# Performance work log

Measured on AMD Instinct MI355X. Metric: run time of the kernel, lower is better.

The kernel has to match this reference:

```python
import jax, jax.numpy as jnp
import numpy as np

ALPHA = 0.1  # history blend factor from __init__


def _grid_sample_border(tex_t, grid):
    """Bilinear grid_sample, align_corners=False, padding_mode='border'.
    tex_t: [N,H,W,C] (channels-last), grid: [N,Hg,Wg,2] with (x,y) in [-1,1].
    Returns [N,Hg,Wg,C].
    """
    N, H, W, C = tex_t.shape
    x = (grid[..., 0] + 1.0) * (W * 0.5) - 0.5  # pixel coords
    y = (grid[..., 1] + 1.0) * (H * 0.5) - 0.5
    x0f = jnp.floor(x)
    y0f = jnp.floor(y)
    wx = (x - x0f)[..., None]
    wy = (y - y0f)[..., None]
    x0 = jnp.clip(x0f.astype(jnp.int32), 0, W - 1)
    x1 = jnp.clip(x0f.astype(jnp.int32) + 1, 0, W - 1)
    y0 = jnp.clip(y0f.astype(jnp.int32), 0, H - 1)
    y1 = jnp.clip(y0f.astype(jnp.int32) + 1, 0, H - 1)
    b = jnp.arange(N)[:, None, None]
    v00 = tex_t[b, y0, x0]
    v01 = tex_t[b, y0, x1]
    v10 = tex_t[b, y1, x0]
    v11 = tex_t[b, y1, x1]
    top = v00 * (1.0 - wx) + v01 * wx
    bot = v10 * (1.0 - wx) + v11 * wx
    return top * (1.0 - wy) + bot * wy


def _bicubic_grid_sample(tex, grid):
    """Catmull-Rom 5-tap bicubic sampling (matches torch BiCubicGridSample).
    tex: [N,C,H,W], grid: [N,Hg,Wg,2]. Returns [N,C,Hg,Wg].
    The torch code appends an all-ones alpha channel before weighting; since
    bilinear sampling of a constant-1 channel is 1, the alpha accumulator
    equals the sum of the 5 scalar weights, which we compute directly.
    """
    N, C, H, W = tex.shape
    tex_t = jnp.transpose(tex, (0, 2, 3, 1))  # NHWC
    ws = jnp.array([W, H], dtype=tex.dtype)
    rws = 1.0 / ws
    uv = (grid + 1.0) * 0.5
    pos = uv * ws
    cpos = jnp.floor(pos - 0.5) + 0.5
    f = pos - cpos
    f2 = f * f
    f3 = f2 * f
    w0 = -0.5 * f3 + f2 - 0.5 * f
    w2 = -1.5 * f3 + 2.0 * f2 + 0.5 * f
    w3 = 0.5 * f3 - 0.5 * f2
    w12 = (1.5 * f3 - 2.5 * f2 + 1.0) + w2  # w1 + w2
    tc12 = rws * (cpos + w2 / w12)
    tc0 = rws * (cpos - 1.0)
    tc3 = rws * (cpos + 2.0)

    def samp(uvx, uvy):
        g = (jnp.stack([uvx, uvy], axis=-1) - 0.5) * 2.0
        return _grid_sample_border(tex_t, g)  # [N,Hg,Wg,C]

    # scalar per-pixel weights
    ww1 = w12[..., 0] * w0[..., 1]
    ww2 = w0[..., 0] * w12[..., 1]
    ww3 = w3[..., 0] * w12[..., 1]
    ww4 = w12[..., 0] * w3[..., 1]
    ww5 = w12[..., 0] * w12[..., 1]

    out = (samp(tc12[..., 0], tc0[..., 1]) * ww1[..., None]
           + samp(tc0[..., 0], tc12[..., 1]) * ww2[..., None]
           + samp(tc3[..., 0], tc12[..., 1]) * ww3[..., None]
           + samp(tc12[..., 0], tc3[..., 1]) * ww4[..., None]
           + samp(tc12[..., 0], tc12[..., 1]) * ww5[..., None])
    rec = (ww1 + ww2 + ww3 + ww4 + ww5)[..., None]
    out = out / rec
    return jnp.transpose(out, (0, 3, 1, 2))  # NCHW


def _max_pool3(x):
    # 3x3 max pool, stride 1, padding 1 on NCHW
    return jax.lax.reduce_window(x, -jnp.inf, jax.lax.max,
                                 (1, 1, 3, 3), (1, 1, 1, 1), 'SAME')


def setup_inputs() -> dict:
    key = jax.random.key(0)
    k1, k2, k3 = jax.random.split(key, 3)
    N, C, H, W = 2, 3, 1080, 1920
    x = jax.random.uniform(k1, (N, C, H, W), dtype=jnp.float32)
    history = jax.random.uniform(k2, (N, C, H, W), dtype=jnp.float32)
    # motion-vector grid: roughly identity UVs with small per-pixel jitter
    gy, gx = jnp.meshgrid(
        (jnp.arange(H, dtype=jnp.float32) + 0.5) / H * 2.0 - 1.0,
        (jnp.arange(W, dtype=jnp.float32) + 0.5) / W * 2.0 - 1.0,
        indexing='ij')
    base = jnp.stack([gx, gy], axis=-1)[None]  # [1,H,W,2]
    jitter = (jax.random.uniform(k3, (N, H, W, 2), dtype=jnp.float32) - 0.5) * 0.01
    mv = base + jitter
    return {"x": x, "mv": mv, "history": history}


def reference(x, mv, history):
    reproj = _bicubic_grid_sample(history, mv)
    max_nh = _max_pool3(x)
    min_nh = -_max_pool3(-x)
    reproj = jnp.minimum(jnp.maximum(reproj, min_nh), max_nh)
    return ALPHA * x + (1.0 - ALPHA) * reproj
```

## Files before the change

kernel.cpp:

```cpp
#include <hip/hip_runtime.h>

static constexpr float ALPHA = 0.1f;

#define TW 64
#define TH 8
#define HROWS 16
#define HCOLS 84
#define CHOFF (HROWS * HCOLS)

__device__ __forceinline__ int iclamp(int v, int lo, int hi) { return min(max(v, lo), hi); }

struct Setup {
    int mA, m1, m2, mB;
    float t, w0, w3, w12;
};

__device__ __forceinline__ Setup axis_setup(float gcoord, float S) {
    Setup s;
    float pos = (gcoord + 1.0f) * 0.5f * S;
    float pm  = floorf(pos - 0.5f);
    float f   = pos - (pm + 0.5f);
    float f2 = f * f, f3 = f2 * f;
    s.w0  = -0.5f * f3 + f2 - 0.5f * f;
    float w2 = -1.5f * f3 + 2.0f * f2 + 0.5f * f;
    s.w3  =  0.5f * f3 - 0.5f * f2;
    s.w12 = (1.5f * f3 - 2.5f * f2 + 1.0f) + w2;
    float p12 = pm + __fdividef(w2, s.w12);
    float fl  = floorf(p12);
    s.t = p12 - fl;
    int m = (int)pm, i12 = (int)fl;
    s.mA = m - 1; s.m1 = i12; s.m2 = i12 + 1; s.mB = m + 2;
    return s;
}

__global__ __launch_bounds__(256, 4) void taa_kernel(
    const float* __restrict__ x, const float* __restrict__ mv,
    const float* __restrict__ hist, float* __restrict__ out)
{
    constexpr int N = 2, H = 1080, W = 1920, HW = H * W;
    constexpr int NTX = W / TW;
    constexpr int NTY = H / TH;
    constexpr int NWG = N * NTX * NTY;
    constexpr int Q = NWG / 8, R = NWG % 8;

    __shared__ __align__(16) float Lh[3 * CHOFF];

    int d = blockIdx.x;
    int xcd = d & 7, di = d >> 3;
    int work = (xcd < R ? xcd * (Q + 1) : R * (Q + 1) + (xcd - R) * Q) + di;
    int n   = work / (NTX * NTY);
    int rem = work - n * (NTX * NTY);
    int ty  = rem / NTX;
    int tx  = rem - ty * NTX;
    const int w0 = tx * TW, h0 = ty * TH;

    const int lx = threadIdx.x & 63;
    const int wv = threadIdx.x >> 6;
    const int wpix = w0 + lx;
    const int hbase = h0 + 2 * wv;

    const float* hn = hist + n * 3 * HW;
    const float* xn = x    + n * 3 * HW;

    const float2 g0 = ((const float2*)mv)[n * HW + hbase * W + wpix];
    const float2 g1 = ((const float2*)mv)[n * HW + (hbase + 1) * W + wpix];

    const bool interior = (tx >= 1) && (tx <= NTX - 2) &&
                          (h0 >= 4) && (h0 + TH + 3 <= H - 1);
    if (interior) {
        float4* Lh4 = (float4*)Lh;
        for (int idx = threadIdx.x; idx < 1008; idx += 256) {
            int c  = idx / 336;
            int rm = idx - c * 336;
            int r  = rm / 21;
            int c4 = rm - r * 21;
            Lh4[idx] = *(const float4*)(hn + c * HW + (h0 - 4 + r) * W + (w0 - 8) + c4 * 4);
        }
    } else {
        for (int idx = threadIdx.x; idx < 4032; idx += 256) {
            int c  = idx / CHOFF;
            int rm = idx - c * CHOFF;
            int r  = rm / HCOLS;
            int cc = rm - r * HCOLS;
            int gr = iclamp(h0 - 4 + r, 0, H - 1);
            int gc = iclamp(w0 - 8 + cc, 0, W - 1);
            Lh[idx] = hn[c * HW + gr * W + gc];
        }
    }

    int rg0 = iclamp(hbase - 1, 0, H - 1) * W;
    int rg1 = hbase * W;
    int rg2 = (hbase + 1) * W;
    int rg3 = iclamp(hbase + 2, 0, H - 1) * W;
    const int rg[4] = {rg0, rg1, rg2, rg3};

    float hmx[3][4], hmn[3][4], xmid[3][4];
    if (tx >= 1 && tx <= NTX - 2) {
#pragma unroll
        for (int c = 0; c < 3; ++c) {
            const float* xc = xn + c * HW + wpix;
#pragma unroll
            for (int rr = 0; rr < 4; ++rr) {
                const float* p = xc + rg[rr];
                float a = p[-1], b = p[0], e = p[1];
                hmx[c][rr]  = fmaxf(fmaxf(a, b), e);
                hmn[c][rr]  = fminf(fminf(a, b), e);
                xmid[c][rr] = b;
            }
        }
    } else {
        const int wm = max(wpix - 1, 0), wp = min(wpix + 1, W - 1);
#pragma unroll
        for (int c = 0; c < 3; ++c) {
            const float* xc = xn + c * HW;
#pragma unroll
            for (int rr = 0; rr < 4; ++rr) {
                float a = xc[rg[rr] + wm];
                float b = xc[rg[rr] + wpix];
                float e = xc[rg[rr] + wp];
                hmx[c][rr]  = fmaxf(fmaxf(a, b), e);
                hmn[c][rr]  = fminf(fminf(a, b), e);
                xmid[c][rr] = b;
            }
        }
    }

    Setup sx0 = axis_setup(g0.x, (float)W);
    Setup sy0 = axis_setup(g0.y, (float)H);
    Setup sx1 = axis_setup(g1.x, (float)W);
    Setup sy1 = axis_setup(g1.y, (float)H);

    __syncthreads();

    float* on = out + n * 3 * HW;

#pragma unroll
    for (int p = 0; p < 2; ++p) {
        const Setup& sx = p ? sx1 : sx0;
        const Setup& sy = p ? sy1 : sy0;

        const int lrA = iclamp(sy.mA - (h0 - 4), 0, HROWS - 1);
        const int lr1 = iclamp(sy.m1 - (h0 - 4), 0, HROWS - 1);
        const int lr2 = iclamp(sy.m2 - (h0 - 4), 0, HROWS - 1);
        const int lrB = iclamp(sy.mB - (h0 - 4), 0, HROWS - 1);
        const int lcA = iclamp(sx.mA - (w0 - 8), 0, HCOLS - 1);
        const int lc1 = iclamp(sx.m1 - (w0 - 8), 0, HCOLS - 1);
        const int lc2 = iclamp(sx.m2 - (w0 - 8), 0, HCOLS - 1);
        const int lcB = iclamp(sx.mB - (w0 - 8), 0, HCOLS - 1);

        const int rA = lrA * HCOLS, r1 = lr1 * HCOLS, r2 = lr2 * HCOLS, rB = lrB * HCOLS;
        const int oA1 = rA + lc1, oA2 = rA + lc2;
        const int o1A = r1 + lcA, o11 = r1 + lc1, o12 = r1 + lc2, o1B = r1 + lcB;
        const int o2A = r2 + lcA, o21 = r2 + lc1, o22 = r2 + lc2, o2B = r2 + lcB;
        const int oB1 = rB + lc1, oB2 = rB + lc2;

        const float tx_ = sx.t, ty_ = sy.t;
        const float omtx = 1.0f - tx_, omty = 1.0f - ty_;
        const float ww1 = sx.w12 * sy.w0;
        const float ww2 = sx.w0  * sy.w12;
        const float ww3 = sx.w3  * sy.w12;
        const float ww4 = sx.w12 * sy.w3;
        const float ww5 = sx.w12 * sy.w12;
        const float rrec = __fdividef(1.0f, ww1 + ww2 + ww3 + ww4 + ww5);

        const int gpix = (hbase + p) * W + wpix;

#pragma unroll
        for (int c = 0; c < 3; ++c) {
            const float* L = Lh + c * CHOFF;
            float s1   = L[oA1] * omtx + L[oA2] * tx_;
            float s4   = L[oB1] * omtx + L[oB2] * tx_;
            float s2   = L[o1A] * omty + L[o2A] * ty_;
            float s3   = L[o1B] * omty + L[o2B] * ty_;
            float top5 = L[o11] * omtx + L[o12] * tx_;
            float bot5 = L[o21] * omtx + L[o22] * tx_;
            float s5   = top5 * omty + bot5 * ty_;
            float reproj = (s1 * ww1 + s2 * ww2 + s3 * ww3 + s4 * ww4 + s5 * ww5) * rrec;

            float mxv = fmaxf(fmaxf(hmx[c][p], hmx[c][p + 1]), hmx[c][p + 2]);
            float mnv = fminf(fminf(hmn[c][p], hmn[c][p + 1]), hmn[c][p + 2]);
            reproj = fminf(fmaxf(reproj, mnv), mxv);

            on[c * HW + gpix] = ALPHA * xmid[c][p + 1] + (1.0f - ALPHA) * reproj;
        }
    }
}

extern "C" void kernel_launch(void* const* d_in, const int* in_sizes, int n_in,
                              void* d_out, int out_size, void* d_ws, size_t ws_size,
                              hipStream_t stream) {
    const float* x    = (const float*)d_in[0];
    const float* mv   = (const float*)d_in[1];
    const float* hist = (const float*)d_in[2];
    float* out = (float*)d_out;

    constexpr int NWG = 2 * (1920 / TW) * (1080 / TH);
    taa_kernel<<<dim3(NWG, 1, 1), dim3(256, 1, 1), 0, stream>>>(x, mv, hist, out);
}
```

Baseline: 48.23 us.

## Interleave history channels in LDS as float4 texels for vectorized gathers

The shared-memory history tile changes from planar per-channel arrays to one padded float4 per texel holding RGB plus a zero. Each bicubic tap then costs one 128-bit LDS read instead of three scalar reads, and the interpolation runs on vectors. The cost is that global loads in the fill loop become scalar, three per texel, instead of float4 row loads. LDS footprint grows by a third for the padding, which may lower occupancy and adds bank pressure on the wide reads.

```diff
diff --git a/kernel.cpp b/kernel.cpp
--- a/kernel.cpp
+++ b/kernel.cpp
@@ -1,12 +1,14 @@
 #include <hip/hip_runtime.h>
 
 static constexpr float ALPHA = 0.1f;
+
+typedef float f4 __attribute__((ext_vector_type(4)));
 
 #define TW 64
 #define TH 8
 #define HROWS 16
 #define HCOLS 84
-#define CHOFF (HROWS * HCOLS)
+#define NTEX (HROWS * HCOLS)
 
 __device__ __forceinline__ int iclamp(int v, int lo, int hi) { return min(max(v, lo), hi); }
 
@@ -43,7 +45,7 @@
     constexpr int NWG = N * NTX * NTY;
     constexpr int Q = NWG / 8, R = NWG % 8;
 
-    __shared__ __align__(16) float Lh[3 * CHOFF];
+    __shared__ __align__(16) f4 Lh[NTEX];
 
     int d = blockIdx.x;
     int xcd = d & 7, di = d >> 3;
@@ -68,23 +70,30 @@
     const bool interior = (tx >= 1) && (tx <= NTX - 2) &&
                           (h0 >= 4) && (h0 + TH + 3 <= H - 1);
     if (interior) {
-        float4* Lh4 = (float4*)Lh;
-        for (int idx = threadIdx.x; idx < 1008; idx += 256) {
-            int c  = idx / 336;
-            int rm = idx - c * 336;
-            int r  = rm / 21;
-            int c4 = rm - r * 21;
-            Lh4[idx] = *(const float4*)(hn + c * HW + (h0 - 4 + r) * W + (w0 - 8) + c4 * 4);
+        for (int idx = threadIdx.x; idx < NTEX; idx += 256) {
+            int r  = idx / HCOLS;
+            int cc = idx - r * HCOLS;
+            const float* src = hn + (h0 - 4 + r) * W + (w0 - 8) + cc;
+            f4 t;
+            t.x = src[0];
+            t.y = src[HW];
+            t.z = src[2 * HW];
+            t.w = 0.0f;
+            Lh[idx] = t;
         }
     } else {
-        for (int idx = threadIdx.x; idx < 4032; idx += 256) {
-            int c  = idx / CHOFF;
-            int rm = idx - c * CHOFF;
-            int r  = rm / HCOLS;
-            int cc = rm - r * HCOLS;
+        for (int idx = threadIdx.x; idx < NTEX; idx += 256) {
+            int r  = idx / HCOLS;
+            int cc = idx - r * HCOLS;
             int gr = iclamp(h0 - 4 + r, 0, H - 1);
             int gc = iclamp(w0 - 8 + cc, 0, W - 1);
-            Lh[idx] = hn[c * HW + gr * W + gc];
+            const float* src = hn + gr * W + gc;
+            f4 t;
+            t.x = src[0];
+            t.y = src[HW];
+            t.z = src[2 * HW];
+            t.w = 0.0f;
+            Lh[idx] = t;
         }
     }
 
@@ -149,10 +158,13 @@
         const int lcB = iclamp(sx.mB - (w0 - 8), 0, HCOLS - 1);
 
         const int rA = lrA * HCOLS, r1 = lr1 * HCOLS, r2 = lr2 * HCOLS, rB = lrB * HCOLS;
-        const int oA1 = rA + lc1, oA2 = rA + lc2;
-        const int o1A = r1 + lcA, o11 = r1 + lc1, o12 = r1 + lc2, o1B = r1 + lcB;
-        const int o2A = r2 + lcA, o21 = r2 + lc1, o22 = r2 + lc2, o2B = r2 + lcB;
-        const int oB1 = rB + lc1, oB2 = rB + lc2;
+
+        f4 tA1 = Lh[rA + lc1], tA2 = Lh[rA + lc2];
+        f4 tB1 = Lh[rB + lc1], tB2 = Lh[rB + lc2];
+        f4 tL1 = Lh[r1 + lcA], tL2 = Lh[r2 + lcA];
+        f4 tR1 = Lh[r1 + lcB], tR2 = Lh[r2 + lcB];
+        f4 tC11 = Lh[r1 + lc1], tC12 = Lh[r1 + lc2];
+        f4 tC21 = Lh[r2 + lc1], tC22 = Lh[r2 + lc2];
 
         const float tx_ = sx.t, ty_ = sy.t;
         const float omtx = 1.0f - tx_, omty = 1.0f - ty_;
@@ -163,24 +175,19 @@
         const float ww5 = sx.w12 * sy.w12;
         const float rrec = __fdividef(1.0f, ww1 + ww2 + ww3 + ww4 + ww5);
 
+        f4 s1 = tA1 * omtx + tA2 * tx_;
+        f4 s4 = tB1 * omtx + tB2 * tx_;
+        f4 s2 = tL1 * omty + tL2 * ty_;
+        f4 s3 = tR1 * omty + tR2 * ty_;
+        f4 s5 = (tC11 * omtx + tC12 * tx_) * omty + (tC21 * omtx + tC22 * tx_) * ty_;
+        f4 rv = (s1 * ww1 + s2 * ww2 + s3 * ww3 + s4 * ww4 + s5 * ww5) * rrec;
+
         const int gpix = (hbase + p) * W + wpix;
-
 #pragma unroll
         for (int c = 0; c < 3; ++c) {
-            const float* L = Lh + c * CHOFF;
-            float s1   = L[oA1] * omtx + L[oA2] * tx_;
-            float s4   = L[oB1] * omtx + L[oB2] * tx_;
-            float s2   = L[o1A] * omty + L[o2A] * ty_;
-            float s3   = L[o1B] * omty + L[o2B] * ty_;
-            float top5 = L[o11] * omtx + L[o12] * tx_;
-            float bot5 = L[o21] * omtx + L[o22] * tx_;
-            float s5   = top5 * omty + bot5 * ty_;
-            float reproj = (s1 * ww1 + s2 * ww2 + s3 * ww3 + s4 * ww4 + s5 * ww5) * rrec;
-
             float mxv = fmaxf(fmaxf(hmx[c][p], hmx[c][p + 1]), hmx[c][p + 2]);
             float mnv = fminf(fminf(hmn[c][p], hmn[c][p + 1]), hmn[c][p + 2]);
-            reproj = fminf(fmaxf(reproj, mnv), mxv);
-
+            float reproj = fminf(fmaxf(rv[c], mnv), mxv);
             on[c * HW + gpix] = ALPHA * xmid[c][p + 1] + (1.0f - ALPHA) * reproj;
         }
     }
```

Measured after the change: 46.06 us. 1.05x faster.
